# Optimization experiments

Measured on AMD Instinct MI355X. Metric: run time of the kernel, lower is better.

The kernel has to match this reference:

```python
import jax, jax.numpy as jnp
import numpy as np

B, S, DIM = 2, 512, 4096
SMAX = 4096
HQ, HKV, HD = 32, 8, 128
REP = HQ // HKV
THETA = 1e6
NEG = -1e9  # stands in for -inf in the causal mask (safe under softmax/vjp)


def setup_inputs() -> dict:
    key = jax.random.key(0)
    ks = jax.random.split(key, 8)
    x = jax.random.normal(ks[0], (B, S, DIM), jnp.float32)
    # RoPE tables (complex freqs_cis represented as cos/sin), rope_theta=1e6
    inv = 1.0 / (THETA ** (np.arange(0, HD, 2, dtype=np.float64) / HD))
    ang = np.arange(SMAX, dtype=np.float64)[:, None] * inv[None, :]
    freqs_cos = jnp.asarray(np.cos(ang), jnp.float32)  # [SMAX, HD//2]
    freqs_sin = jnp.asarray(np.sin(ang), jnp.float32)
    cache = jax.random.normal(ks[1], (2, 1, B, SMAX, HKV, HD), jnp.float32) * 0.02
    i = np.arange(SMAX)
    mask = jnp.asarray(np.where(i[None, :] <= i[:, None], 0.0, NEG), jnp.float32)
    storage_idx = jnp.arange(S, dtype=jnp.int32)
    sc = 0.02
    wq = jax.random.normal(ks[2], (HQ * HD, DIM), jnp.float32) * sc
    wk = jax.random.normal(ks[3], (HKV * HD, DIM), jnp.float32) * sc
    wv = jax.random.normal(ks[4], (HKV * HD, DIM), jnp.float32) * sc
    wo = jax.random.normal(ks[5], (DIM, HQ * HD), jnp.float32) * sc
    return {"x": x, "freqs_cos": freqs_cos, "freqs_sin": freqs_sin, "cache": cache,
            "mask": mask, "storage_idx": storage_idx, "wq": wq, "wk": wk, "wv": wv, "wo": wo}


def _rope(t, c, s):
    # t: [B,S,H,HD]; consecutive pairs (2i, 2i+1) form complex numbers
    tr = t.reshape(*t.shape[:-1], -1, 2)
    a, b = tr[..., 0], tr[..., 1]
    o0 = a * c - b * s
    o1 = a * s + b * c
    return jnp.stack([o0, o1], axis=-1).reshape(t.shape)


def reference(x, freqs_cos, freqs_sin, cache, mask, storage_idx, wq, wk, wv, wo):
    bsz, seqlen, _ = x.shape
    hd = cache.shape[-1]
    hkv = cache.shape[-2]
    hq = wq.shape[0] // hd
    rep = hq // hkv
    xq = (x @ wq.T).reshape(bsz, seqlen, hq, hd)
    xk = (x @ wk.T).reshape(bsz, seqlen, hkv, hd)
    xv = (x @ wv.T).reshape(bsz, seqlen, hkv, hd)
    c = freqs_cos[storage_idx][None, :, None, :]  # [1,S,1,HD//2]
    s = freqs_sin[storage_idx][None, :, None, :]
    xq = _rope(xq, c, s)
    xk = _rope(xk, c, s)
    # rotating-cache write (index_copy along seq dim of cache[0/1, li])
    k_cache = cache[0, 0].at[:, storage_idx].set(xk)  # [B,SMAX,HKV,HD]
    v_cache = cache[1, 0].at[:, storage_idx].set(xv)
    keys = jnp.repeat(k_cache, rep, axis=2)    # GQA expand -> [B,SMAX,HQ,HD]
    values = jnp.repeat(v_cache, rep, axis=2)
    # NOTE: faithful to source: scores = QK^T / (head_dim ** -0.5)
    scores = jnp.einsum('bqhd,bkhd->bhqk', xq, keys) / (hd ** -0.5)
    scores = scores + mask[storage_idx][None, None, :, :]
    probs = jax.nn.softmax(scores.astype(jnp.float32), axis=-1).astype(xq.dtype)
    out = jnp.einsum('bhqk,bkhd->bqhd', probs, values).reshape(bsz, seqlen, hq * hd)
    return out @ wo.T
```

## Files before the change

kernel.cpp:

```cpp
#include <hip/hip_runtime.h>

#define Bn   2
#define Sn   512
#define DIMn 4096
#define HQn  32
#define HKVn 8
#define HDn  128
#define NPAIR 64
#define KVN  (HKVn * HDn)
#define NALL (DIMn + 2 * KVN)
#define SCALE 11.313708498984761f

typedef short bf16x8 __attribute__((ext_vector_type(8)));
typedef float f32x4 __attribute__((ext_vector_type(4)));
typedef unsigned short ushort8 __attribute__((ext_vector_type(8)));
typedef signed char char8 __attribute__((ext_vector_type(8)));
typedef int i32x4 __attribute__((ext_vector_type(4)));

__device__ __forceinline__ unsigned short f2bf_rne(float f) {
  unsigned u = __builtin_bit_cast(unsigned, f);
  u += 0x7fffu + ((u >> 16) & 1u);
  return (unsigned short)(u >> 16);
}
__device__ __forceinline__ float bf2f(unsigned short h) {
  unsigned u = ((unsigned)h) << 16;
  return __builtin_bit_cast(float, u);
}
__device__ __forceinline__ void split_bf16(float x, unsigned short& hi, unsigned short& lo) {
  unsigned u = __builtin_bit_cast(unsigned, x);
  hi = (unsigned short)(u >> 16);
  float hf = __builtin_bit_cast(float, u & 0xffff0000u);
  lo = (unsigned short)(__builtin_bit_cast(unsigned, x - hf) >> 16);
}
__device__ __forceinline__ void gload16(const void* g, void* lds) {
  __builtin_amdgcn_global_load_lds(
      (const __attribute__((address_space(1))) unsigned int*)g,
      (__attribute__((address_space(3))) unsigned int*)lds, 16, 0, 0);
}

__global__ __launch_bounds__(256) void quant_rows(
    const float* __restrict__ x, const float* __restrict__ wq,
    const float* __restrict__ wk, const float* __restrict__ wv,
    const float* __restrict__ wo,
    signed char* __restrict__ xh8, signed char* __restrict__ xl8,
    signed char* __restrict__ wh8, signed char* __restrict__ wl8,
    signed char* __restrict__ wo8,
    float* __restrict__ sA, float* __restrict__ sW, float* __restrict__ sWo,
    unsigned* __restrict__ amaxp)
{
  const int r = blockIdx.x;
  const int t = threadIdx.x;
  if (r == 0 && t == 0) *amaxp = 0u;

  __shared__ float wm[4];

  if (r >= 1024 + NALL) {
    int wr2 = r - 1024 - NALL;
    const float* src = wo + (size_t)wr2 * DIMn;
    float4 v[4];
    float am = 0.f;
    #pragma unroll
    for (int j = 0; j < 4; ++j) {
      v[j] = ((const float4*)src)[t + j * 256];
      am = fmaxf(am, fmaxf(fmaxf(fabsf(v[j].x), fabsf(v[j].y)),
                           fmaxf(fabsf(v[j].z), fabsf(v[j].w))));
    }
    #pragma unroll
    for (int o = 1; o < 64; o <<= 1) am = fmaxf(am, __shfl_xor(am, o));
    if ((t & 63) == 0) wm[t >> 6] = am;
    __syncthreads();
    am = fmaxf(fmaxf(wm[0], wm[1]), fmaxf(wm[2], wm[3]));
    const float inv = (am > 0.f) ? 127.0f / am : 0.f;
    if (t == 0) sWo[wr2] = am * (1.0f / 127.0f);
    signed char* dst = wo8 + (size_t)wr2 * DIMn;
    #pragma unroll
    for (int j = 0; j < 4; ++j) {
      float fv[4] = {v[j].x, v[j].y, v[j].z, v[j].w};
      char4 q;
      q.x = (signed char)__float2int_rn(fv[0] * inv);
      q.y = (signed char)__float2int_rn(fv[1] * inv);
      q.z = (signed char)__float2int_rn(fv[2] * inv);
      q.w = (signed char)__float2int_rn(fv[3] * inv);
      ((char4*)dst)[t + j * 256] = q;
    }
    return;
  }

  const float* src; signed char* ph; signed char* pl; float* ps; size_t prow;
  if (r < 1024) {
    src = x + (size_t)r * DIMn; ph = xh8; pl = xl8; ps = sA + r; prow = (size_t)r * DIMn;
  } else {
    int wr_ = r - 1024;
    ps = sW + wr_; ph = wh8; pl = wl8; prow = (size_t)wr_ * DIMn;
    if (wr_ < DIMn)            src = wq + (size_t)wr_ * DIMn;
    else if (wr_ < DIMn + KVN) src = wk + (size_t)(wr_ - DIMn) * DIMn;
    else                       src = wv + (size_t)(wr_ - DIMn - KVN) * DIMn;
  }
  float4 v[4];
  float am = 0.f;
  #pragma unroll
  for (int j = 0; j < 4; ++j) {
    v[j] = ((const float4*)src)[t + j * 256];
    am = fmaxf(am, fmaxf(fmaxf(fabsf(v[j].x), fabsf(v[j].y)),
                         fmaxf(fabsf(v[j].z), fabsf(v[j].w))));
  }
  #pragma unroll
  for (int o = 1; o < 64; o <<= 1) am = fmaxf(am, __shfl_xor(am, o));
  if ((t & 63) == 0) wm[t >> 6] = am;
  __syncthreads();
  am = fmaxf(fmaxf(wm[0], wm[1]), fmaxf(wm[2], wm[3]));
  const float inv = (am > 0.f) ? 32512.0f / am : 0.f;
  if (t == 0) *ps = am * (1.0f / 32512.0f);
  #pragma unroll
  for (int j = 0; j < 4; ++j) {
    float fv[4] = {v[j].x, v[j].y, v[j].z, v[j].w};
    signed char hh[4], ll[4];
    #pragma unroll
    for (int e = 0; e < 4; ++e) {
      int q = __float2int_rn(fv[e] * inv);
      int hi = (q + 128) >> 8;
      hh[e] = (signed char)hi;
      ll[e] = (signed char)(q - (hi << 8));
    }
    ((char4*)(ph + prow))[t + j * 256] = make_char4(hh[0], hh[1], hh[2], hh[3]);
    ((char4*)(pl + prow))[t + j * 256] = make_char4(ll[0], ll[1], ll[2], ll[3]);
  }
}

__global__ __launch_bounds__(256) void aquant_k(
    const unsigned short* __restrict__ Aw, signed char* __restrict__ A8,
    const unsigned* __restrict__ amaxp, int n8)
{
  const float am = __builtin_bit_cast(float, *amaxp);
  const float inv = (am > 0.f) ? 127.0f / am : 0.f;
  int i = blockIdx.x * blockDim.x + threadIdx.x;
  if (i >= n8) return;
  ushort8 a = ((const ushort8*)Aw)[i];
  char8 q;
  #pragma unroll
  for (int j = 0; j < 8; ++j)
    q[j] = (signed char)__float2int_rn(bf2f(a[j]) * inv);
  ((char8*)A8)[i] = q;
}

__global__ __launch_bounds__(256, 2) void qkv_gemm_i8(
    const signed char* __restrict__ Ah, const signed char* __restrict__ Al,
    const signed char* __restrict__ Wh, const signed char* __restrict__ Wl,
    const float* __restrict__ sA, const float* __restrict__ sW,
    float* __restrict__ CQ, float* __restrict__ CK, unsigned short* __restrict__ CV)
{
  constexpr int KS = 64;
  constexpr int TILEB = 224 * 128;
  __shared__ __align__(16) signed char Ls[2][TILEB];

  const int t = threadIdx.x, w = t >> 6, lane = t & 63;
  const int bid = blockIdx.x;
  const int s = (bid & 7) * 64 + (bid >> 3);
  const int bx = s >> 3, by = s & 7;
  const int bm = by * 128, bn = bx * 96;

  const signed char* gsrc[7];
  int ldst[7];
  #pragma unroll
  for (int j = 0; j < 4; ++j) {
    int u = j * 256 + t;
    int R = u >> 3, slot = u & 7;
    int q = slot ^ (R & 7);
    gsrc[j] = (q < 4 ? Ah : Al) + (size_t)(bm + R) * DIMn + (q & 3) * 16;
    ldst[j] = u * 16;
  }
  #pragma unroll
  for (int j = 4; j < 7; ++j) {
    int base0 = (j - 4) * 16;
    int rb = base0 + (t >> 3) + ((t < 128) ? 0 : 32);
    int slot = t & 7;
    int q = slot ^ (rb & 7);
    gsrc[j] = (q < 4 ? Wh : Wl) + (size_t)(bn + rb) * DIMn + (q & 3) * 16;
    ldst[j] = (128 + rb) * 128 + slot * 16;
  }

  const int wr = w >> 1, wc = w & 1;
  const int rl = lane & 15, kh = lane >> 4;
  int aoff[4], boff[3];
  #pragma unroll
  for (int fm = 0; fm < 4; ++fm) {
    int R = wr * 64 + fm * 16 + rl;
    aoff[fm] = R * 128 + ((kh ^ (R & 7)) * 16);
  }
  #pragma unroll
  for (int fn = 0; fn < 3; ++fn) {
    int R = 128 + wc * 48 + fn * 16 + rl;
    boff[fn] = R * 128 + ((kh ^ (R & 7)) * 16);
  }

  i32x4 acc1[4][3], acc2[4][3];
  #pragma unroll
  for (int i = 0; i < 4; ++i)
  #pragma unroll
    for (int j = 0; j < 3; ++j) {
      acc1[i][j] = (i32x4){0, 0, 0, 0};
      acc2[i][j] = (i32x4){0, 0, 0, 0};
    }

  const int nt = DIMn / KS;
  #pragma unroll
  for (int j = 0; j < 7; ++j) gload16(gsrc[j], &Ls[0][ldst[j]]);

  for (int tt = 0; tt < nt; ++tt) {
    const int buf = tt & 1, nbuf = buf ^ 1;
    const bool more = (tt + 1 < nt);
    const signed char* Lp = &Ls[buf][0];
    i32x4 ah[4], al[4];

    asm volatile("s_waitcnt vmcnt(2)" ::: "memory");
    __builtin_amdgcn_s_barrier();
    __builtin_amdgcn_sched_barrier(0);
    if (more) {
      #pragma unroll
      for (int j = 0; j < 5; ++j)
        gload16(gsrc[j] + (size_t)(tt + 1) * KS, &Ls[nbuf][ldst[j]]);
    }
    #pragma unroll
    for (int fm = 0; fm < 4; ++fm) {
      ah[fm] = *(const i32x4*)(Lp + aoff[fm]);
      al[fm] = *(const i32x4*)(Lp + (aoff[fm] ^ 64));
    }
    {
      i32x4 bh = *(const i32x4*)(Lp + boff[0]);
      i32x4 bl = *(const i32x4*)(Lp + (boff[0] ^ 64));
      __builtin_amdgcn_s_setprio(1);
      #pragma unroll
      for (int fm = 0; fm < 4; ++fm) {
        acc1[fm][0] = __builtin_amdgcn_mfma_i32_16x16x64_i8(ah[fm], bh, acc1[fm][0], 0, 0, 0);
        acc2[fm][0] = __builtin_amdgcn_mfma_i32_16x16x64_i8(ah[fm], bl, acc2[fm][0], 0, 0, 0);
        acc2[fm][0] = __builtin_amdgcn_mfma_i32_16x16x64_i8(al[fm], bh, acc2[fm][0], 0, 0, 0);
      }
      __builtin_amdgcn_s_setprio(0);
    }

    if (more) asm volatile("s_waitcnt vmcnt(6)" ::: "memory");
    else      asm volatile("s_waitcnt vmcnt(1)" ::: "memory");
    __builtin_amdgcn_s_barrier();
    __builtin_amdgcn_sched_barrier(0);
    if (more)
      gload16(gsrc[5] + (size_t)(tt + 1) * KS, &Ls[nbuf][ldst[5]]);
    {
      i32x4 bh = *(const i32x4*)(Lp + boff[1]);
      i32x4 bl = *(const i32x4*)(Lp + (boff[1] ^ 64));
      __builtin_amdgcn_s_setprio(1);
      #pragma unroll
      for (int fm = 0; fm < 4; ++fm) {
        acc1[fm][1] = __builtin_amdgcn_mfma_i32_16x16x64_i8(ah[fm], bh, acc1[fm][1], 0, 0, 0);
        acc2[fm][1] = __builtin_amdgcn_mfma_i32_16x16x64_i8(ah[fm], bl, acc2[fm][1], 0, 0, 0);
        acc2[fm][1] = __builtin_amdgcn_mfma_i32_16x16x64_i8(al[fm], bh, acc2[fm][1], 0, 0, 0);
      }
      __builtin_amdgcn_s_setprio(0);
    }

    if (more) asm volatile("s_waitcnt vmcnt(6)" ::: "memory");
    else      asm volatile("s_waitcnt vmcnt(0)" ::: "memory");
    __builtin_amdgcn_s_barrier();
    __builtin_amdgcn_sched_barrier(0);
    if (more)
      gload16(gsrc[6] + (size_t)(tt + 1) * KS, &Ls[nbuf][ldst[6]]);
    {
      i32x4 bh = *(const i32x4*)(Lp + boff[2]);
      i32x4 bl = *(const i32x4*)(Lp + (boff[2] ^ 64));
      __builtin_amdgcn_s_setprio(1);
      #pragma unroll
      for (int fm = 0; fm < 4; ++fm) {
        acc1[fm][2] = __builtin_amdgcn_mfma_i32_16x16x64_i8(ah[fm], bh, acc1[fm][2], 0, 0, 0);
        acc2[fm][2] = __builtin_amdgcn_mfma_i32_16x16x64_i8(ah[fm], bl, acc2[fm][2], 0, 0, 0);
        acc2[fm][2] = __builtin_amdgcn_mfma_i32_16x16x64_i8(al[fm], bh, acc2[fm][2], 0, 0, 0);
      }
      __builtin_amdgcn_s_setprio(0);
    }
  }

  #pragma unroll
  for (int fn = 0; fn < 3; ++fn) {
    const int colW = bn + wc * 48 + fn * 16 + rl;
    const float sw = sW[colW];
    #pragma unroll
    for (int fm = 0; fm < 4; ++fm) {
      #pragma unroll
      for (int j = 0; j < 4; ++j) {
        int grow = bm + wr * 64 + fm * 16 + kh * 4 + j;
        float val = sA[grow] * sw *
            fmaf((float)acc1[fm][fn][j], 65536.0f, (float)acc2[fm][fn][j] * 256.0f);
        if (colW < DIMn)            CQ[(size_t)grow * DIMn + colW] = val;
        else if (colW < DIMn + KVN) CK[(size_t)grow * KVN + (colW - DIMn)] = val;
        else                        CV[(size_t)grow * KVN + (colW - DIMn - KVN)] = f2bf_rne(val);
      }
    }
  }
}

__global__ __launch_bounds__(256, 2) void oproj_i8(
    const signed char* __restrict__ A8, const signed char* __restrict__ Wo8,
    const float* __restrict__ sWo, const unsigned* __restrict__ amaxp,
    float* __restrict__ out)
{
  constexpr int KS = 128;
  constexpr int TILEB = 192 * 128;
  __shared__ __align__(16) signed char Ls[3 * TILEB];

  const int t = threadIdx.x, w = t >> 6, lane = t & 63;
  const int bid = blockIdx.x;
  const int s = (bid & 7) * 64 + (bid >> 3);
  const int bm = (s & 7) * 128, bn = (s >> 3) * 64;

  const signed char* gsrc[6];
  #pragma unroll
  for (int j = 0; j < 6; ++j) {
    int u = j * 256 + t;
    int R = u >> 3, slot = u & 7;
    int q = slot ^ (R & 7);
    const signed char* base = (R < 128) ? A8 : Wo8;
    int rg = (R < 128) ? (bm + R) : (bn + (R - 128));
    gsrc[j] = base + (size_t)rg * DIMn + q * 16;
  }

  const int wr = w >> 1, wc = w & 1;
  const int rl = lane & 15, kh = lane >> 4;
  int aoff[4], boff[2];
  #pragma unroll
  for (int fm = 0; fm < 4; ++fm) {
    int R = wr * 64 + fm * 16 + rl;
    aoff[fm] = R * 128 + ((kh ^ (R & 7)) * 16);
  }
  #pragma unroll
  for (int fn = 0; fn < 2; ++fn) {
    int R = 128 + wc * 32 + fn * 16 + rl;
    boff[fn] = R * 128 + ((kh ^ (R & 7)) * 16);
  }

  i32x4 acc[4][2];
  #pragma unroll
  for (int i = 0; i < 4; ++i)
  #pragma unroll
    for (int j = 0; j < 2; ++j) acc[i][j] = (i32x4){0, 0, 0, 0};

  const int nt = DIMn / KS;
  #pragma unroll
  for (int j = 0; j < 6; ++j) gload16(gsrc[j], &Ls[0 * TILEB + (j * 256 + t) * 16]);
  #pragma unroll
  for (int j = 0; j < 6; ++j) gload16(gsrc[j] + KS, &Ls[1 * TILEB + (j * 256 + t) * 16]);

  int cur = 0;
  for (int tt = 0; tt < nt; ++tt) {
    if (tt + 1 < nt) asm volatile("s_waitcnt vmcnt(6)" ::: "memory");
    else             asm volatile("s_waitcnt vmcnt(0)" ::: "memory");
    __builtin_amdgcn_s_barrier();
    __builtin_amdgcn_sched_barrier(0);

    int pre = cur + 2; if (pre >= 3) pre -= 3;
    if (tt + 2 < nt) {
      #pragma unroll
      for (int j = 0; j < 6; ++j)
        gload16(gsrc[j] + (size_t)(tt + 2) * KS, &Ls[pre * TILEB + (j * 256 + t) * 16]);
    }

    const signed char* Lp = &Ls[cur * TILEB];
    i32x4 a0[4], a1[4], b0[2], b1[2];
    #pragma unroll
    for (int fm = 0; fm < 4; ++fm) {
      a0[fm] = *(const i32x4*)(Lp + aoff[fm]);
      a1[fm] = *(const i32x4*)(Lp + (aoff[fm] ^ 64));
    }
    #pragma unroll
    for (int fn = 0; fn < 2; ++fn) {
      b0[fn] = *(const i32x4*)(Lp + boff[fn]);
      b1[fn] = *(const i32x4*)(Lp + (boff[fn] ^ 64));
    }
    __builtin_amdgcn_s_setprio(1);
    #pragma unroll
    for (int fm = 0; fm < 4; ++fm)
    #pragma unroll
      for (int fn = 0; fn < 2; ++fn) {
        acc[fm][fn] = __builtin_amdgcn_mfma_i32_16x16x64_i8(a0[fm], b0[fn], acc[fm][fn], 0, 0, 0);
        acc[fm][fn] = __builtin_amdgcn_mfma_i32_16x16x64_i8(a1[fm], b1[fn], acc[fm][fn], 0, 0, 0);
      }
    __builtin_amdgcn_s_setprio(0);
    cur += 1; if (cur >= 3) cur -= 3;
  }

  const float sAg = __builtin_bit_cast(float, *amaxp) * (1.0f / 127.0f);
  const int crow0 = bm + wr * 64 + kh * 4;
  #pragma unroll
  for (int fn = 0; fn < 2; ++fn) {
    const int col = bn + wc * 32 + fn * 16 + rl;
    const float sw = sWo[col] * sAg;
    #pragma unroll
    for (int fm = 0; fm < 4; ++fm)
    #pragma unroll
      for (int j = 0; j < 4; ++j)
        out[(size_t)(crow0 + fm * 16 + j) * DIMn + col] = sw * (float)acc[fm][fn][j];
  }
}

template<bool SPLIT, int BN>
__global__ __launch_bounds__(256, 2) void gemm_mfma(
    const float* __restrict__ A,
    const float* __restrict__ W0, float* __restrict__ C0,
    const float* __restrict__ W1, float* __restrict__ C1,
    int Kd, int N)
{
  constexpr int BM = 64;
  constexpr int KSTEP = SPLIT ? 32 : 64;
  constexpr int CPR = SPLIT ? 4 : 8;
  constexpr int AUNITS = BM * KSTEP / 8;
  constexpr int UNITS  = (BM + BN) * KSTEP / 8;
  constexpr int UPT = UNITS / 256;
  constexpr int FN = BN / 32;
  constexpr int ROWS = BM + BN;

  __shared__ __align__(16) unsigned short Ls[2][ROWS * 64];

  const float* __restrict__ W = (blockIdx.z == 0) ? W0 : W1;
  float* __restrict__ Cp = (blockIdx.z == 0) ? C0 : C1;

  const int t  = threadIdx.x;
  const int bm = blockIdx.y * BM;
  const int bn = blockIdx.x * BN;

  const float* gsrc[UPT];
  int loff[UPT];
  #pragma unroll
  for (int i = 0; i < UPT; ++i) {
    int u = i * 256 + t;
    int row, c;
    if (u < AUNITS) {
      row = u / CPR; c = u % CPR;
      gsrc[i] = A + (size_t)(bm + row) * Kd + c * 8;
    } else {
      int v = u - AUNITS;
      int rr = v / CPR; c = v % CPR;
      row = BM + rr;
      gsrc[i] = W + (size_t)(bn + rr) * Kd + c * 8;
    }
    loff[i] = row * 64 + (c ^ (row & 7)) * 8;
  }

  const int lane = t & 63;
  const int w  = t >> 6;
  const int wr = w >> 1, wc = w & 1;
  const int rl = lane & 15, kh = lane >> 4;

  int aoff[2], boff[FN];
  #pragma unroll
  for (int fm = 0; fm < 2; ++fm) {
    int row = wr * 32 + fm * 16 + rl;
    aoff[fm] = row * 64 + (kh ^ (row & 7)) * 8;
  }
  #pragma unroll
  for (int fn = 0; fn < FN; ++fn) {
    int row = BM + wc * (BN / 2) + fn * 16 + rl;
    boff[fn] = row * 64 + (kh ^ (row & 7)) * 8;
  }

  f32x4 acc[2][FN];
  #pragma unroll
  for (int i = 0; i < 2; ++i)
  #pragma unroll
    for (int j = 0; j < FN; ++j) acc[i][j] = (f32x4){0.f, 0.f, 0.f, 0.f};

  float4 f0[UPT], f1[UPT];
  #pragma unroll
  for (int i = 0; i < UPT; ++i) {
    f0[i] = *(const float4*)(gsrc[i]);
    f1[i] = *(const float4*)(gsrc[i] + 4);
  }

  const int nt = Kd / KSTEP;
  for (int tt = 0; tt < nt; ++tt) {
    unsigned short* Lp = &Ls[tt & 1][0];
    #pragma unroll
    for (int i = 0; i < UPT; ++i) {
      float xv[8] = {f0[i].x, f0[i].y, f0[i].z, f0[i].w,
                     f1[i].x, f1[i].y, f1[i].z, f1[i].w};
      ushort8 hi, lo;
      #pragma unroll
      for (int j = 0; j < 8; ++j) {
        if constexpr (SPLIT) {
          unsigned short h_, l_;
          split_bf16(xv[j], h_, l_);
          hi[j] = h_; lo[j] = l_;
        } else {
          hi[j] = f2bf_rne(xv[j]);
          lo[j] = 0;
        }
      }
      *(ushort8*)(Lp + loff[i]) = hi;
      if constexpr (SPLIT)
        *(ushort8*)(((uintptr_t)(Lp + loff[i])) ^ 64) = lo;
    }
    if (tt + 1 < nt) {
      #pragma unroll
      for (int i = 0; i < UPT; ++i) {
        f0[i] = *(const float4*)(gsrc[i] + (size_t)(tt + 1) * KSTEP);
        f1[i] = *(const float4*)(gsrc[i] + (size_t)(tt + 1) * KSTEP + 4);
      }
    }
    __syncthreads();

    bf16x8 a0[2], a1[2], b0[FN], b1[FN];
    #pragma unroll
    for (int fm = 0; fm < 2; ++fm) {
      const unsigned short* p = Lp + aoff[fm];
      a0[fm] = *(const bf16x8*)p;
      a1[fm] = *(const bf16x8*)(((uintptr_t)p) ^ 64);
    }
    #pragma unroll
    for (int fn = 0; fn < FN; ++fn) {
      const unsigned short* p = Lp + boff[fn];
      b0[fn] = *(const bf16x8*)p;
      b1[fn] = *(const bf16x8*)(((uintptr_t)p) ^ 64);
    }
    #pragma unroll
    for (int fm = 0; fm < 2; ++fm)
    #pragma unroll
      for (int fn = 0; fn < FN; ++fn) {
        if constexpr (SPLIT) {
          acc[fm][fn] = __builtin_amdgcn_mfma_f32_16x16x32_bf16(a0[fm], b0[fn], acc[fm][fn], 0, 0, 0);
          acc[fm][fn] = __builtin_amdgcn_mfma_f32_16x16x32_bf16(a1[fm], b0[fn], acc[fm][fn], 0, 0, 0);
          acc[fm][fn] = __builtin_amdgcn_mfma_f32_16x16x32_bf16(a0[fm], b1[fn], acc[fm][fn], 0, 0, 0);
        } else {
          acc[fm][fn] = __builtin_amdgcn_mfma_f32_16x16x32_bf16(a0[fm], b0[fn], acc[fm][fn], 0, 0, 0);
          acc[fm][fn] = __builtin_amdgcn_mfma_f32_16x16x32_bf16(a1[fm], b1[fn], acc[fm][fn], 0, 0, 0);
        }
      }
  }

  const int crow0 = bm + wr * 32 + kh * 4;
  const int ccol0 = bn + wc * (BN / 2) + rl;
  #pragma unroll
  for (int fm = 0; fm < 2; ++fm)
  #pragma unroll
    for (int fn = 0; fn < FN; ++fn)
    #pragma unroll
      for (int j = 0; j < 4; ++j)
        Cp[(size_t)(crow0 + fm * 16 + j) * N + ccol0 + fn * 16] = acc[fm][fn][j];
}

#define KT 32

template<bool BF16IO, bool AMAX>
__global__ __launch_bounds__(256, 2) void flash_attn_mfma(
    const float* __restrict__ Qg, const float* __restrict__ Kg, const void* __restrict__ Vgv,
    const float* __restrict__ fc, const float* __restrict__ fs,
    const int* __restrict__ sidx, void* __restrict__ Ov, unsigned* __restrict__ amaxp)
{
  const int bid = blockIdx.x;
  const int qt = bid & 7;
  const int h  = (bid >> 3) & 31;
  const int b  = bid >> 8;
  const int q0 = qt * 64;
  const int hk = h >> 2;

  __shared__ __align__(16) unsigned short Ks[2][2][32][128];
  __shared__ __align__(16) unsigned short Vt[2][128][40];
  __shared__ float wmx[4];

  const int t = threadIdx.x;
  const int w = t >> 6;
  const int lane = t & 63;
  const int rl = lane & 15;
  const int kh = lane >> 4;

  const int qrow = q0 + w * 16 + rl;
  const int qp = sidx[qrow];

  int kr[2], kc_[2];
  #pragma unroll
  for (int i = 0; i < 2; ++i) { int u = i * 256 + t; kr[i] = u >> 4; kc_[i] = u & 15; }
  const int kkv = t >> 3, dcv = t & 7;

  const int nkt = (q0 + 64) / KT;
  const int qmaxw = q0 + w * 16 + 15;

  float kreg[2][8]; float4 kc4[2], ks4[2];
  float vregf[16];
  ushort8 vregu[2];

  #pragma unroll
  for (int i = 0; i < 2; ++i) {
    const float* kp_ = Kg + ((size_t)(b * Sn + kr[i]) * HKVn + hk) * HDn + kc_[i] * 8;
    *(float4*)&kreg[i][0] = *(const float4*)kp_;
    *(float4*)&kreg[i][4] = *(const float4*)(kp_ + 4);
    int posk = sidx[kr[i]];
    kc4[i] = *(const float4*)(fc + (size_t)posk * NPAIR + kc_[i] * 4);
    ks4[i] = *(const float4*)(fs + (size_t)posk * NPAIR + kc_[i] * 4);
  }
  if constexpr (BF16IO) {
    const unsigned short* vp_ = (const unsigned short*)Vgv +
        ((size_t)(b * Sn + kkv) * HKVn + hk) * HDn + dcv * 16;
    vregu[0] = *(const ushort8*)vp_;
    vregu[1] = *(const ushort8*)(vp_ + 8);
  } else {
    const float* vp_ = (const float*)Vgv + ((size_t)(b * Sn + kkv) * HKVn + hk) * HDn + dcv * 16;
    #pragma unroll
    for (int i = 0; i < 4; ++i) *(float4*)&vregf[i * 4] = *(const float4*)(vp_ + i * 4);
  }

  bf16x8 qh[4], ql[4];
  {
    const float* qptr = Qg + ((size_t)(b * Sn + qrow) * HQn + h) * HDn;
    #pragma unroll
    for (int ds = 0; ds < 4; ++ds) {
      int d0 = ds * 32 + kh * 8;
      float4 u0 = *(const float4*)(qptr + d0);
      float4 u1 = *(const float4*)(qptr + d0 + 4);
      float4 c4 = *(const float4*)(fc + (size_t)qp * NPAIR + d0 / 2);
      float4 s4 = *(const float4*)(fs + (size_t)qp * NPAIR + d0 / 2);
      float v[8];
      v[0] = u0.x * c4.x - u0.y * s4.x;  v[1] = u0.x * s4.x + u0.y * c4.x;
      v[2] = u0.z * c4.y - u0.w * s4.y;  v[3] = u0.z * s4.y + u0.w * c4.y;
      v[4] = u1.x * c4.z - u1.y * s4.z;  v[5] = u1.x * s4.z + u1.y * c4.z;
      v[6] = u1.z * c4.w - u1.w * s4.w;  v[7] = u1.z * s4.w + u1.w * c4.w;
      #pragma unroll
      for (int j = 0; j < 8; ++j) {
        unsigned short h_, l_;
        split_bf16(v[j], h_, l_);
        qh[ds][j] = (short)h_; ql[ds][j] = (short)l_;
      }
    }
  }

  float m_run = -3.0e38f, l_run = 0.f;
  f32x4 acc_o[8];
  #pragma unroll
  for (int i = 0; i < 8; ++i) acc_o[i] = (f32x4){0.f, 0.f, 0.f, 0.f};

  for (int tt = 0; tt < nkt; ++tt) {
    const int kbase = tt * KT;
    const int buf = tt & 1;

    #pragma unroll
    for (int i = 0; i < 2; ++i) {
      float rv[8];
      rv[0] = kreg[i][0] * kc4[i].x - kreg[i][1] * ks4[i].x;
      rv[1] = kreg[i][0] * ks4[i].x + kreg[i][1] * kc4[i].x;
      rv[2] = kreg[i][2] * kc4[i].y - kreg[i][3] * ks4[i].y;
      rv[3] = kreg[i][2] * ks4[i].y + kreg[i][3] * kc4[i].y;
      rv[4] = kreg[i][4] * kc4[i].z - kreg[i][5] * ks4[i].z;
      rv[5] = kreg[i][4] * ks4[i].z + kreg[i][5] * kc4[i].z;
      rv[6] = kreg[i][6] * kc4[i].w - kreg[i][7] * ks4[i].w;
      rv[7] = kreg[i][6] * ks4[i].w + kreg[i][7] * kc4[i].w;
      ushort8 hi, lo;
      #pragma unroll
      for (int j = 0; j < 8; ++j) {
        unsigned short h_, l_;
        split_bf16(rv[j], h_, l_);
        hi[j] = h_; lo[j] = l_;
      }
      int slot = kc_[i] ^ (kr[i] & 15);
      *(ushort8*)&Ks[buf][0][kr[i]][slot * 8] = hi;
      *(ushort8*)&Ks[buf][1][kr[i]][slot * 8] = lo;
    }
    if constexpr (BF16IO) {
      #pragma unroll
      for (int i = 0; i < 8; ++i) {
        Vt[buf][dcv * 16 + i][kkv] = vregu[0][i];
        Vt[buf][dcv * 16 + 8 + i][kkv] = vregu[1][i];
      }
    } else {
      #pragma unroll
      for (int i = 0; i < 16; ++i)
        Vt[buf][dcv * 16 + i][kkv] = f2bf_rne(vregf[i]);
    }

    if (tt + 1 < nkt) {
      const int kb = kbase + KT;
      #pragma unroll
      for (int i = 0; i < 2; ++i) {
        const float* kp_ = Kg + ((size_t)(b * Sn + kb + kr[i]) * HKVn + hk) * HDn + kc_[i] * 8;
        *(float4*)&kreg[i][0] = *(const float4*)kp_;
        *(float4*)&kreg[i][4] = *(const float4*)(kp_ + 4);
        int posk = sidx[kb + kr[i]];
        kc4[i] = *(const float4*)(fc + (size_t)posk * NPAIR + kc_[i] * 4);
        ks4[i] = *(const float4*)(fs + (size_t)posk * NPAIR + kc_[i] * 4);
      }
      if constexpr (BF16IO) {
        const unsigned short* vp_ = (const unsigned short*)Vgv +
            ((size_t)(b * Sn + kb + kkv) * HKVn + hk) * HDn + dcv * 16;
        vregu[0] = *(const ushort8*)vp_;
        vregu[1] = *(const ushort8*)(vp_ + 8);
      } else {
        const float* vp_ = (const float*)Vgv + ((size_t)(b * Sn + kb + kkv) * HKVn + hk) * HDn + dcv * 16;
        #pragma unroll
        for (int i = 0; i < 4; ++i) *(float4*)&vregf[i * 4] = *(const float4*)(vp_ + i * 4);
      }
    }
    __syncthreads();

    if (kbase > qmaxw) continue;

    float p[8];
    #pragma unroll
    for (int fm = 0; fm < 2; ++fm) {
      f32x4 accs = (f32x4){0.f, 0.f, 0.f, 0.f};
      #pragma unroll
      for (int ds = 0; ds < 4; ++ds) {
        int slot = (ds * 4 + kh) ^ rl;
        bf16x8 kH = *(const bf16x8*)&Ks[buf][0][fm * 16 + rl][slot * 8];
        bf16x8 kL = *(const bf16x8*)&Ks[buf][1][fm * 16 + rl][slot * 8];
        accs = __builtin_amdgcn_mfma_f32_16x16x32_bf16(kH, qh[ds], accs, 0, 0, 0);
        accs = __builtin_amdgcn_mfma_f32_16x16x32_bf16(kL, qh[ds], accs, 0, 0, 0);
        accs = __builtin_amdgcn_mfma_f32_16x16x32_bf16(kH, ql[ds], accs, 0, 0, 0);
      }
      #pragma unroll
      for (int r = 0; r < 4; ++r) {
        int kp = kbase + fm * 16 + kh * 4 + r;
        p[fm * 4 + r] = accs[r] * SCALE + ((kp <= qp) ? 0.f : -1.0e9f);
      }
    }

    float tmax = p[0];
    #pragma unroll
    for (int i = 1; i < 8; ++i) tmax = fmaxf(tmax, p[i]);
    tmax = fmaxf(tmax, __shfl_xor(tmax, 16));
    tmax = fmaxf(tmax, __shfl_xor(tmax, 32));
    float m_new = fmaxf(m_run, tmax);
    float crs = __expf(m_run - m_new);
    m_run = m_new;
    float tsum = 0.f;
    bf16x8 pa;
    #pragma unroll
    for (int i = 0; i < 8; ++i) {
      float ev = __expf(p[i] - m_new);
      tsum += ev;
      pa[i] = (short)f2bf_rne(ev);
    }
    tsum += __shfl_xor(tsum, 16);
    tsum += __shfl_xor(tsum, 32);
    l_run = l_run * crs + tsum;

    float cq[4];
    #pragma unroll
    for (int r = 0; r < 4; ++r) cq[r] = __shfl(crs, kh * 4 + r);

    #pragma unroll
    for (int db = 0; db < 8; ++db) {
      short4 v0 = *(const short4*)&Vt[buf][db * 16 + rl][kh * 4];
      short4 v1 = *(const short4*)&Vt[buf][db * 16 + rl][16 + kh * 4];
      bf16x8 vb = {v0.x, v0.y, v0.z, v0.w, v1.x, v1.y, v1.z, v1.w};
      f32x4 a = acc_o[db];
      a[0] *= cq[0]; a[1] *= cq[1]; a[2] *= cq[2]; a[3] *= cq[3];
      acc_o[db] = __builtin_amdgcn_mfma_f32_16x16x32_bf16(pa, vb, a, 0, 0, 0);
    }
  }

  float lq[4];
  #pragma unroll
  for (int r = 0; r < 4; ++r) lq[r] = 1.0f / __shfl(l_run, kh * 4 + r);
  float lmax = 0.f;
  #pragma unroll
  for (int db = 0; db < 8; ++db)
  #pragma unroll
    for (int r = 0; r < 4; ++r) {
      int q = q0 + w * 16 + kh * 4 + r;
      size_t idx = ((size_t)(b * Sn + q) * HQn + h) * HDn + db * 16 + rl;
      float val = acc_o[db][r] * lq[r];
      if constexpr (AMAX) lmax = fmaxf(lmax, fabsf(val));
      if constexpr (BF16IO) ((unsigned short*)Ov)[idx] = f2bf_rne(val);
      else                  ((float*)Ov)[idx] = val;
    }
  if constexpr (AMAX) {
    #pragma unroll
    for (int o = 1; o < 64; o <<= 1) lmax = fmaxf(lmax, __shfl_xor(lmax, o));
    if (lane == 0) wmx[w] = lmax;
    __syncthreads();
    if (t == 0) {
      float m = fmaxf(fmaxf(wmx[0], wmx[1]), fmaxf(wmx[2], wmx[3]));
      atomicMax(amaxp, __builtin_bit_cast(unsigned, m));
    }
  }
}

extern "C" void kernel_launch(void* const* d_in, const int* in_sizes, int n_in,
                              void* d_out, int out_size, void* d_ws, size_t ws_size,
                              hipStream_t stream)
{
  const float* x    = (const float*)d_in[0];
  const float* fc   = (const float*)d_in[1];
  const float* fs   = (const float*)d_in[2];
  const int*   sidx = (const int*)d_in[5];
  const float* wq   = (const float*)d_in[6];
  const float* wk   = (const float*)d_in[7];
  const float* wv   = (const float*)d_in[8];
  const float* wo   = (const float*)d_in[9];
  float* out = (float*)d_out;

  const int M = Bn * Sn;
  const size_t EX  = (size_t)M * DIMn;
  const size_t EW  = (size_t)DIMn * DIMn;
  const size_t EK  = (size_t)M * KVN;
  const size_t EW8 = (size_t)NALL * DIMn;

  char* p = (char*)d_ws;
  signed char* xh8 = (signed char*)p;        p += EX;
  signed char* xl8 = (signed char*)p;        p += EX;
  signed char* wh8 = (signed char*)p;        p += EW8;
  signed char* wl8 = (signed char*)p;        p += EW8;
  signed char* wo8 = (signed char*)p;        p += EW;
  signed char* A8  = (signed char*)p;        p += EX;
  float* sA  = (float*)p;                    p += 1024 * 4;
  float* sW  = (float*)p;                    p += (size_t)NALL * 4;
  float* sWo = (float*)p;                    p += (size_t)DIMn * 4;
  unsigned* amaxp = (unsigned*)p;            p += 256;
  float* Qw = (float*)p;                     p += 4 * EX;
  float* Kw = (float*)p;                     p += 4 * EK;
  unsigned short* Vw = (unsigned short*)p;   p += 2 * EK;
  unsigned short* Aw = (unsigned short*)p;   p += 2 * EX;
  const size_t NEED = (size_t)(p - (char*)d_ws);

  if (ws_size >= NEED) {
    quant_rows<<<1024 + NALL + DIMn, 256, 0, stream>>>(
        x, wq, wk, wv, wo, xh8, xl8, wh8, wl8, wo8, sA, sW, sWo, amaxp);
    qkv_gemm_i8<<<512, 256, 0, stream>>>(
        xh8, xl8, wh8, wl8, sA, sW, Qw, Kw, Vw);
    flash_attn_mfma<true, true><<<Bn * HQn * (Sn / 64), 256, 0, stream>>>(
        Qw, Kw, Vw, fc, fs, sidx, Aw, amaxp);
    aquant_k<<<(int)(EX / 8 / 256), 256, 0, stream>>>(Aw, A8, amaxp, (int)(EX / 8));
    oproj_i8<<<512, 256, 0, stream>>>(A8, wo8, sWo, amaxp, out);
  } else {
    float* Qw2 = (float*)d_ws;
    float* Kw2 = Qw2 + (size_t)M * HQn * HDn;
    float* Vw2 = Kw2 + (size_t)M * HKVn * HDn;
    float* Aw2 = Vw2 + (size_t)M * HKVn * HDn;
    unsigned* dummyA = (unsigned*)(Aw2 + (size_t)M * HQn * HDn);
    gemm_mfma<true, 128><<<dim3(DIMn / 128, M / 64, 1), 256, 0, stream>>>(
        x, wq, Qw2, wq, Qw2, DIMn, DIMn);
    gemm_mfma<true, 64><<<dim3((HKVn * HDn) / 64, M / 64, 2), 256, 0, stream>>>(
        x, wk, Kw2, wv, Vw2, DIMn, HKVn * HDn);
    flash_attn_mfma<false, false><<<Bn * HQn * (Sn / 64), 256, 0, stream>>>(
        Qw2, Kw2, Vw2, fc, fs, sidx, Aw2, dummyA);
    gemm_mfma<false, 128><<<dim3(DIMn / 128, M / 64, 1), 256, 0, stream>>>(
        Aw2, wo, out, wo, out, DIMn, DIMn);
  }
}
```

Before: 199.9 us.

## Fuse attention-output int8 quantization into flash epilogue using V amax bound

The scale for the attention output is now derived from the absolute max of V, computed in the QKV GEMM epilogue. Softmax output is a convex combination of V rows, so max|V| bounds the output. This lets the flash-attention kernel quantize its output straight to int8. That removes the separate aquant kernel, the bf16 intermediate buffer write and read, and the per-block amax reduction and atomic in attention. In exchange the scale is coarser, so int8 quantization of the attention output loses some precision. The V-column GEMM blocks also gain an extra reduction, barrier and atomic.

```diff
diff --git a/kernel.cpp b/kernel.cpp
--- a/kernel.cpp
+++ b/kernel.cpp
@@ -127,31 +127,17 @@
   }
 }
 
-__global__ __launch_bounds__(256) void aquant_k(
-    const unsigned short* __restrict__ Aw, signed char* __restrict__ A8,
-    const unsigned* __restrict__ amaxp, int n8)
-{
-  const float am = __builtin_bit_cast(float, *amaxp);
-  const float inv = (am > 0.f) ? 127.0f / am : 0.f;
-  int i = blockIdx.x * blockDim.x + threadIdx.x;
-  if (i >= n8) return;
-  ushort8 a = ((const ushort8*)Aw)[i];
-  char8 q;
-  #pragma unroll
-  for (int j = 0; j < 8; ++j)
-    q[j] = (signed char)__float2int_rn(bf2f(a[j]) * inv);
-  ((char8*)A8)[i] = q;
-}
-
 __global__ __launch_bounds__(256, 2) void qkv_gemm_i8(
     const signed char* __restrict__ Ah, const signed char* __restrict__ Al,
     const signed char* __restrict__ Wh, const signed char* __restrict__ Wl,
     const float* __restrict__ sA, const float* __restrict__ sW,
-    float* __restrict__ CQ, float* __restrict__ CK, unsigned short* __restrict__ CV)
+    float* __restrict__ CQ, float* __restrict__ CK, unsigned short* __restrict__ CV,
+    unsigned* __restrict__ amaxp)
 {
   constexpr int KS = 64;
   constexpr int TILEB = 224 * 128;
   __shared__ __align__(16) signed char Ls[2][TILEB];
+  __shared__ float redx[4];
 
   const int t = threadIdx.x, w = t >> 6, lane = t & 63;
   const int bid = blockIdx.x;
@@ -277,6 +263,7 @@
     }
   }
 
+  float vmax = 0.f;
   #pragma unroll
   for (int fn = 0; fn < 3; ++fn) {
     const int colW = bn + wc * 48 + fn * 16 + rl;
@@ -290,8 +277,21 @@
             fmaf((float)acc1[fm][fn][j], 65536.0f, (float)acc2[fm][fn][j] * 256.0f);
         if (colW < DIMn)            CQ[(size_t)grow * DIMn + colW] = val;
         else if (colW < DIMn + KVN) CK[(size_t)grow * KVN + (colW - DIMn)] = val;
-        else                        CV[(size_t)grow * KVN + (colW - DIMn - KVN)] = f2bf_rne(val);
-      }
+        else {
+          CV[(size_t)grow * KVN + (colW - DIMn - KVN)] = f2bf_rne(val);
+          vmax = fmaxf(vmax, fabsf(val));
+        }
+      }
+    }
+  }
+  if (bn + 96 > DIMn + KVN) {
+    #pragma unroll
+    for (int o = 1; o < 64; o <<= 1) vmax = fmaxf(vmax, __shfl_xor(vmax, o));
+    if (lane == 0) redx[w] = vmax;
+    __syncthreads();
+    if (t == 0) {
+      float m = fmaxf(fmaxf(redx[0], redx[1]), fmaxf(redx[2], redx[3]));
+      if (m > 0.f) atomicMax(amaxp, __builtin_bit_cast(unsigned, m));
     }
   }
 }
@@ -545,11 +545,12 @@
 
 #define KT 32
 
-template<bool BF16IO, bool AMAX>
+template<bool I8OUT>
 __global__ __launch_bounds__(256, 2) void flash_attn_mfma(
     const float* __restrict__ Qg, const float* __restrict__ Kg, const void* __restrict__ Vgv,
     const float* __restrict__ fc, const float* __restrict__ fs,
-    const int* __restrict__ sidx, void* __restrict__ Ov, unsigned* __restrict__ amaxp)
+    const int* __restrict__ sidx, void* __restrict__ Ov,
+    const unsigned* __restrict__ amaxp)
 {
   const int bid = blockIdx.x;
   const int qt = bid & 7;
@@ -560,7 +561,6 @@
 
   __shared__ __align__(16) unsigned short Ks[2][2][32][128];
   __shared__ __align__(16) unsigned short Vt[2][128][40];
-  __shared__ float wmx[4];
 
   const int t = threadIdx.x;
   const int w = t >> 6;
@@ -592,7 +592,7 @@
     kc4[i] = *(const float4*)(fc + (size_t)posk * NPAIR + kc_[i] * 4);
     ks4[i] = *(const float4*)(fs + (size_t)posk * NPAIR + kc_[i] * 4);
   }
-  if constexpr (BF16IO) {
+  if constexpr (I8OUT) {
     const unsigned short* vp_ = (const unsigned short*)Vgv +
         ((size_t)(b * Sn + kkv) * HKVn + hk) * HDn + dcv * 16;
     vregu[0] = *(const ushort8*)vp_;
@@ -658,7 +658,7 @@
       *(ushort8*)&Ks[buf][0][kr[i]][slot * 8] = hi;
       *(ushort8*)&Ks[buf][1][kr[i]][slot * 8] = lo;
     }
-    if constexpr (BF16IO) {
+    if constexpr (I8OUT) {
       #pragma unroll
       for (int i = 0; i < 8; ++i) {
         Vt[buf][dcv * 16 + i][kkv] = vregu[0][i];
@@ -681,7 +681,7 @@
         kc4[i] = *(const float4*)(fc + (size_t)posk * NPAIR + kc_[i] * 4);
         ks4[i] = *(const float4*)(fs + (size_t)posk * NPAIR + kc_[i] * 4);
       }
-      if constexpr (BF16IO) {
+      if constexpr (I8OUT) {
         const unsigned short* vp_ = (const unsigned short*)Vgv +
             ((size_t)(b * Sn + kb + kkv) * HKVn + hk) * HDn + dcv * 16;
         vregu[0] = *(const ushort8*)vp_;
@@ -754,7 +754,11 @@
   float lq[4];
   #pragma unroll
   for (int r = 0; r < 4; ++r) lq[r] = 1.0f / __shfl(l_run, kh * 4 + r);
-  float lmax = 0.f;
+  float qinv = 0.f;
+  if constexpr (I8OUT) {
+    const float amv = __builtin_bit_cast(float, *amaxp);
+    qinv = (amv > 0.f) ? 127.0f / amv : 0.f;
+  }
   #pragma unroll
   for (int db = 0; db < 8; ++db)
   #pragma unroll
@@ -762,20 +766,14 @@
       int q = q0 + w * 16 + kh * 4 + r;
       size_t idx = ((size_t)(b * Sn + q) * HQn + h) * HDn + db * 16 + rl;
       float val = acc_o[db][r] * lq[r];
-      if constexpr (AMAX) lmax = fmaxf(lmax, fabsf(val));
-      if constexpr (BF16IO) ((unsigned short*)Ov)[idx] = f2bf_rne(val);
-      else                  ((float*)Ov)[idx] = val;
-    }
-  if constexpr (AMAX) {
-    #pragma unroll
-    for (int o = 1; o < 64; o <<= 1) lmax = fmaxf(lmax, __shfl_xor(lmax, o));
-    if (lane == 0) wmx[w] = lmax;
-    __syncthreads();
-    if (t == 0) {
-      float m = fmaxf(fmaxf(wmx[0], wmx[1]), fmaxf(wmx[2], wmx[3]));
-      atomicMax(amaxp, __builtin_bit_cast(unsigned, m));
-    }
-  }
+      if constexpr (I8OUT) {
+        int qv = __float2int_rn(val * qinv);
+        qv = qv > 127 ? 127 : (qv < -127 ? -127 : qv);
+        ((signed char*)Ov)[idx] = (signed char)qv;
+      } else {
+        ((float*)Ov)[idx] = val;
+      }
+    }
 }
 
 extern "C" void kernel_launch(void* const* d_in, const int* in_sizes, int n_in,
@@ -812,17 +810,15 @@
   float* Qw = (float*)p;                     p += 4 * EX;
   float* Kw = (float*)p;                     p += 4 * EK;
   unsigned short* Vw = (unsigned short*)p;   p += 2 * EK;
-  unsigned short* Aw = (unsigned short*)p;   p += 2 * EX;
   const size_t NEED = (size_t)(p - (char*)d_ws);
 
   if (ws_size >= NEED) {
     quant_rows<<<1024 + NALL + DIMn, 256, 0, stream>>>(
         x, wq, wk, wv, wo, xh8, xl8, wh8, wl8, wo8, sA, sW, sWo, amaxp);
     qkv_gemm_i8<<<512, 256, 0, stream>>>(
-        xh8, xl8, wh8, wl8, sA, sW, Qw, Kw, Vw);
-    flash_attn_mfma<true, true><<<Bn * HQn * (Sn / 64), 256, 0, stream>>>(
-        Qw, Kw, Vw, fc, fs, sidx, Aw, amaxp);
-    aquant_k<<<(int)(EX / 8 / 256), 256, 0, stream>>>(Aw, A8, amaxp, (int)(EX / 8));
+        xh8, xl8, wh8, wl8, sA, sW, Qw, Kw, Vw, amaxp);
+    flash_attn_mfma<true><<<Bn * HQn * (Sn / 64), 256, 0, stream>>>(
+        Qw, Kw, Vw, fc, fs, sidx, A8, amaxp);
     oproj_i8<<<512, 256, 0, stream>>>(A8, wo8, sWo, amaxp, out);
   } else {
     float* Qw2 = (float*)d_ws;
@@ -834,7 +830,7 @@
         x, wq, Qw2, wq, Qw2, DIMn, DIMn);
     gemm_mfma<true, 64><<<dim3((HKVn * HDn) / 64, M / 64, 2), 256, 0, stream>>>(
         x, wk, Kw2, wv, Vw2, DIMn, HKVn * HDn);
-    flash_attn_mfma<false, false><<<Bn * HQn * (Sn / 64), 256, 0, stream>>>(
+    flash_attn_mfma<false><<<Bn * HQn * (Sn / 64), 256, 0, stream>>>(
         Qw2, Kw2, Vw2, fc, fs, sidx, Aw2, dummyA);
     gemm_mfma<false, 128><<<dim3(DIMn / 128, M / 64, 1), 256, 0, stream>>>(
         Aw2, wo, out, wo, out, DIMn, DIMn);
```

Result: no change. 198.6 us (-0.7%).
